# Kernel optimization log

Hardware: AMD Instinct MI355X
Metric: run time of the kernel (lower is better)

## Reference

```python
import jax, jax.numpy as jnp
import numpy as np

N = 100000
IN_DIM = 1280
HID = 128
EPS = 1e-5

def _gconv(x, src, dst, W, b, n):
    # DGL GraphConv, norm='both': D_out^{-1/2} gather -> sum -> D_in^{-1/2}, then W, b.
    # Project first (in_feats >= out_feats here) so edge messages are HID-dim.
    ones = jnp.ones(src.shape[0], dtype=x.dtype)
    out_deg = jnp.clip(jax.ops.segment_sum(ones, src, num_segments=n), 1.0)
    in_deg = jnp.clip(jax.ops.segment_sum(ones, dst, num_segments=n), 1.0)
    h = (x * (out_deg ** -0.5)[:, None]) @ W          # [n, HID]
    agg = jax.ops.segment_sum(h[src], dst, num_segments=n)  # scatter-add over edges
    return agg * (in_deg ** -0.5)[:, None] + b

def _batchnorm(x, g, b):
    m = x.mean(0)
    v = jnp.mean((x - m) ** 2, axis=0)  # biased variance (torch BN normalization)
    return (x - m) * jax.lax.rsqrt(v + EPS) * g + b

def _layer(x, edges, W, b, fcW, fcb, g, beta, n):
    # HeteroGraphConv aggregate='sum' over 3 relations, then FC + ReLU + BN
    h = _gconv(x, edges[0][0], edges[0][1], W[0], b[0], n)
    h = h + _gconv(x, edges[1][0], edges[1][1], W[1], b[1], n)
    h = h + _gconv(x, edges[2][0], edges[2][1], W[2], b[2], n)
    h = h @ fcW + fcb
    h = jax.nn.relu(h)
    return _batchnorm(h, g, beta)

def setup_inputs() -> dict:
    key = jax.random.key(0)
    ks = jax.random.split(key, 16)
    x = jax.random.normal(ks[0], (N, IN_DIM), dtype=jnp.float32)
    seq_edges = jax.random.randint(ks[1], (2, 200000), 0, N, dtype=jnp.int32)
    knn_edges = jax.random.randint(ks[2], (2, 1000000), 0, N, dtype=jnp.int32)
    dis_edges = jax.random.randint(ks[3], (2, 1600000), 0, N, dtype=jnp.int32)
    s_in = 1.0 / np.sqrt(IN_DIM)
    s_h = 1.0 / np.sqrt(HID)
    W0 = jax.random.normal(ks[4], (3, IN_DIM, HID), dtype=jnp.float32) * s_in
    b0 = jnp.zeros((3, HID), dtype=jnp.float32)
    fcW0 = jax.random.normal(ks[5], (HID, HID), dtype=jnp.float32) * s_h
    fcb0 = jnp.zeros((HID,), dtype=jnp.float32)
    g0 = jnp.ones((HID,), dtype=jnp.float32)
    beta0 = jnp.zeros((HID,), dtype=jnp.float32)
    W1 = jax.random.normal(ks[6], (3, HID, HID), dtype=jnp.float32) * s_h
    b1 = jnp.zeros((3, HID), dtype=jnp.float32)
    fcW1 = jax.random.normal(ks[7], (HID, HID), dtype=jnp.float32) * s_h
    fcb1 = jnp.zeros((HID,), dtype=jnp.float32)
    g1 = jnp.ones((HID,), dtype=jnp.float32)
    beta1 = jnp.zeros((HID,), dtype=jnp.float32)
    return {"x": x, "seq_edges": seq_edges, "knn_edges": knn_edges, "dis_edges": dis_edges,
            "W0": W0, "b0": b0, "fcW0": fcW0, "fcb0": fcb0, "g0": g0, "beta0": beta0,
            "W1": W1, "b1": b1, "fcW1": fcW1, "fcb1": fcb1, "g1": g1, "beta1": beta1}

def reference(x, seq_edges, knn_edges, dis_edges,
              W0, b0, fcW0, fcb0, g0, beta0,
              W1, b1, fcW1, fcb1, g1, beta1):
    edges = [seq_edges, knn_edges, dis_edges]
    n = x.shape[0]
    h = _layer(x, edges, W0, b0, fcW0, fcb0, g0, beta0, n)
    # dropout after non-final layers is identity at eval
    h = _layer(h, edges, W1, b1, fcW1, fcb1, g1, beta1, n)
    return h
```

## Files before the change

### kernel.cpp

```cpp
#include <hip/hip_runtime.h>
#include <hip/hip_bf16.h>
#include <math.h>

#define NN 100000
#define HID 128
#define EPSV 1e-5f

typedef short bf16x8 __attribute__((ext_vector_type(8)));
typedef float f32x4 __attribute__((ext_vector_type(4)));
typedef unsigned short u16;

__device__ __forceinline__ u16 f2b(float f) {
  unsigned u = __builtin_bit_cast(unsigned, f);
  u += 0x7FFFu + ((u >> 16) & 1u);
  return (u16)(u >> 16);
}
__device__ __forceinline__ float b2f(u16 h) {
  unsigned u = ((unsigned)h) << 16;
  return __builtin_bit_cast(float, u);
}

#define AS1(p) ((__attribute__((address_space(1))) void*)(p))
#define AS3(p) ((__attribute__((address_space(3))) void*)(p))


static __global__ void k_zero(float* __restrict__ p, int n) {
  int i = blockIdx.x * blockDim.x + threadIdx.x;
  if (i < n) p[i] = 0.f;
}

static __global__ void k_zero_i(int* __restrict__ p, int n) {
  int i = blockIdx.x * blockDim.x + threadIdx.x;
  if (i < n) p[i] = 0;
}

static __global__ void k_deg(const int* __restrict__ src, const int* __restrict__ dst,
                             int E, float* __restrict__ outdeg, float* __restrict__ indeg) {
  int e = blockIdx.x * blockDim.x + threadIdx.x;
  if (e < E) {
    atomicAdd(&outdeg[src[e]], 1.f);
    atomicAdd(&indeg[dst[e]], 1.f);
  }
}

static __global__ void k_counts(const float* __restrict__ indegRaw, int* __restrict__ counts, int n3) {
  int i = blockIdx.x * blockDim.x + threadIdx.x;
  if (i < n3) counts[i] = (int)indegRaw[i];
  else if (i == n3) counts[i] = 0;
}

static __global__ void k_rsqrt_clip(float* __restrict__ p, int n) {
  int i = blockIdx.x * blockDim.x + threadIdx.x;
  if (i < n) p[i] = rsqrtf(fmaxf(p[i], 1.f));
}

static __global__ void k_scan1(const int* __restrict__ in, int* __restrict__ out,
                               int* __restrict__ aux, int n) {
  __shared__ int s[256];
  int t = threadIdx.x, i = blockIdx.x * 256 + t;
  int v = (i < n) ? in[i] : 0;
  s[t] = v; __syncthreads();
#pragma unroll
  for (int d = 1; d < 256; d <<= 1) {
    int x = (t >= d) ? s[t - d] : 0;
    __syncthreads();
    s[t] += x;
    __syncthreads();
  }
  if (i < n) out[i] = s[t] - v;
  if (t == 255) aux[blockIdx.x] = s[255];
}

static __global__ void k_scan2(int* __restrict__ aux, int nb) {
  __shared__ int s[256];
  __shared__ int carry;
  int t = threadIdx.x;
  if (t == 0) carry = 0;
  __syncthreads();
  for (int base = 0; base < nb; base += 256) {
    int i = base + t;
    int v = (i < nb) ? aux[i] : 0;
    s[t] = v; __syncthreads();
#pragma unroll
    for (int d = 1; d < 256; d <<= 1) {
      int x = (t >= d) ? s[t - d] : 0;
      __syncthreads();
      s[t] += x;
      __syncthreads();
    }
    int excl = s[t] - v + carry;
    if (i < nb) aux[i] = excl;
    int tot = s[255];
    __syncthreads();
    if (t == 0) carry += tot;
    __syncthreads();
  }
}

static __global__ void k_scan3(int* __restrict__ out, const int* __restrict__ aux, int n) {
  int i = blockIdx.x * 256 + threadIdx.x;
  if (i < n) out[i] += aux[blockIdx.x];
}

static __global__ void k_fill(const int* __restrict__ src, const int* __restrict__ dst, int E,
                              const int* __restrict__ off, int* __restrict__ cur,
                              int rbase, int* __restrict__ srt) {
  int e = blockIdx.x * blockDim.x + threadIdx.x;
  if (e < E) {
    int d = dst[e];
    int p = off[rbase + d] + atomicAdd(&cur[rbase + d], 1);
    srt[p] = src[e];
  }
}

static __global__ void k_cvt_w(const float* __restrict__ W, u16* __restrict__ Wt, int K) {
  int i = blockIdx.x * blockDim.x + threadIdx.x;
  int tot = 3 * K * 128;
  if (i < tot) {
    int rel = i / (K * 128);
    int rem = i - rel * K * 128;
    int k = rem >> 7;
    int c = rem & 127;
    Wt[((size_t)rel * 128 + c) * K + k] = f2b(W[i]);
  }
}

static __global__ void k_cvt_fcw(const float* __restrict__ W, u16* __restrict__ Bt) {
  int i = blockIdx.x * blockDim.x + threadIdx.x;
  if (i < 128 * 128) {
    int k = i >> 7, c = i & 127;
    Bt[c * 128 + k] = f2b(W[i]);
  }
}

template<int K, bool AF32>
__global__ __launch_bounds__(256, 3)
void k_gemm2p(const void* __restrict__ Av,
              const u16* __restrict__ Wt,
              const float* __restrict__ sout,
              u16* __restrict__ Y,
              int M, int NT)
{
  constexpr int A_U16 = AF32 ? 8192 : 4096;
  constexpr int B_U16 = 4096;
  __shared__ u16 lds[2][A_U16 + B_U16];

  const int bid  = blockIdx.x;
  const int xcd  = bid & 7;
  const int s    = bid >> 3;
  const int rel  = s % 3;
  const int tile = xcd + 8 * (s / 3);
  if (tile >= NT) return;
  const int row0 = tile * 128;

  const int t    = threadIdx.x;
  const int lane = t & 63;
  const int w    = t >> 6;
  const int wm   = w >> 1, wn = w & 1;
  const int l15  = lane & 15, l4 = lane >> 4;
  const int kl   = l4 * 8;
  const int nk   = K / 32;

  const u16* Wr = Wt + (size_t)rel * 128 * K;

  int r0 = row0 + (2 * w) * 16 + l15;      if (r0 >= M) r0 = M - 1;
  int r1 = row0 + (2 * w + 1) * 16 + l15;  if (r1 >= M) r1 = M - 1;

  const u16* gb0 = Wr + (size_t)((2 * w) * 16 + l15) * K + kl;
  const u16* gb1 = Wr + (size_t)((2 * w + 1) * 16 + l15) * K + kl;

  const float* Af = (const float*)Av;
  const u16*   Ab = (const u16*)Av;

  auto STAGE = [&](int buf, int k0) {
    u16* L = &lds[buf][0];
    if constexpr (AF32) {
      const float* sa0 = Af + (size_t)r0 * K + k0 + kl;
      const float* sa1 = Af + (size_t)r1 * K + k0 + kl;
      __builtin_amdgcn_global_load_lds(AS1(sa0),     AS3(L + (2 * w) * 1024),       16, 0, 0);
      __builtin_amdgcn_global_load_lds(AS1(sa0 + 4), AS3(L + (2 * w) * 1024 + 512), 16, 0, 0);
      __builtin_amdgcn_global_load_lds(AS1(sa1),     AS3(L + (2 * w + 1) * 1024),       16, 0, 0);
      __builtin_amdgcn_global_load_lds(AS1(sa1 + 4), AS3(L + (2 * w + 1) * 1024 + 512), 16, 0, 0);
    } else {
      const u16* sa0 = Ab + (size_t)r0 * K + k0 + kl;
      const u16* sa1 = Ab + (size_t)r1 * K + k0 + kl;
      __builtin_amdgcn_global_load_lds(AS1(sa0), AS3(L + (2 * w) * 512),     16, 0, 0);
      __builtin_amdgcn_global_load_lds(AS1(sa1), AS3(L + (2 * w + 1) * 512), 16, 0, 0);
    }
    u16* Bd = L + A_U16;
    __builtin_amdgcn_global_load_lds(AS1(gb0 + k0), AS3(Bd + (2 * w) * 512),     16, 0, 0);
    __builtin_amdgcn_global_load_lds(AS1(gb1 + k0), AS3(Bd + (2 * w + 1) * 512), 16, 0, 0);
  };

  f32x4 acc[4][4];
#pragma unroll
  for (int m = 0; m < 4; ++m)
#pragma unroll
    for (int n = 0; n < 4; ++n) acc[m][n] = (f32x4){0.f, 0.f, 0.f, 0.f};

  STAGE(0, 0);

  for (int k = 0; k < nk; ++k) {
    asm volatile("s_waitcnt vmcnt(0)" ::: "memory");
    __builtin_amdgcn_sched_barrier(0);
    __builtin_amdgcn_s_barrier();
    __builtin_amdgcn_sched_barrier(0);

    if (k + 1 < nk) STAGE((k + 1) & 1, (k + 1) * 32);

    const int cur = k & 1;
    bf16x8 a[4], b[4];
    if constexpr (AF32) {
      const float* Al = (const float*)&lds[cur][0];
#pragma unroll
      for (int m = 0; m < 4; ++m) {
        f32x4 lo = *(const f32x4*)&Al[(wm * 4 + m) * 512 + lane * 4];
        f32x4 hi = *(const f32x4*)&Al[(wm * 4 + m) * 512 + 256 + lane * 4];
        union { bf16x8 v; u16 u[8]; } q;
#pragma unroll
        for (int j = 0; j < 4; ++j) {
          q.u[j]     = __builtin_bit_cast(u16, __float2bfloat16(lo[j]));
          q.u[4 + j] = __builtin_bit_cast(u16, __float2bfloat16(hi[j]));
        }
        a[m] = q.v;
      }
    } else {
      const u16* Al = &lds[cur][0];
#pragma unroll
      for (int m = 0; m < 4; ++m) a[m] = *(const bf16x8*)&Al[(wm * 4 + m) * 512 + lane * 8];
    }
    {
      const u16* Bl = &lds[cur][A_U16];
#pragma unroll
      for (int n = 0; n < 4; ++n) b[n] = *(const bf16x8*)&Bl[(wn * 4 + n) * 512 + lane * 8];
    }

#pragma unroll
    for (int m = 0; m < 4; ++m)
#pragma unroll
      for (int n = 0; n < 4; ++n)
        acc[m][n] = __builtin_amdgcn_mfma_f32_16x16x32_bf16(a[m], b[n], acc[m][n], 0, 0, 0);
  }

#pragma unroll
  for (int m = 0; m < 4; ++m) {
    const int rb = row0 + wm * 64 + m * 16 + l4 * 4;
#pragma unroll
    for (int j = 0; j < 4; ++j) {
      const int row = rb + j;
      if (row < M) {
        const float sc = sout[(size_t)rel * NN + row];
        u16* yp = Y + (size_t)row * 384 + rel * 128 + wn * 64 + l15;
#pragma unroll
        for (int n = 0; n < 4; ++n) yp[n * 16] = f2b(acc[m][n][j] * sc);
      }
    }
  }
}

static __global__ __launch_bounds__(256)
void k_gather(const int* __restrict__ off, const int* __restrict__ srt,
              const float* __restrict__ sin_, const u16* __restrict__ Y,
              const float* __restrict__ b, u16* __restrict__ acc16)
{
  int d = blockIdx.x * 4 + (threadIdx.x >> 6);
  if (d >= NN) return;
  int c = (threadIdx.x & 63) * 2;
  float v0 = b[c]     + b[128 + c]     + b[256 + c];
  float v1 = b[c + 1] + b[128 + c + 1] + b[256 + c + 1];
#pragma unroll
  for (int r = 0; r < 3; ++r) {
    int base = r * NN + d;
    int j0 = off[base], j1 = off[base + 1];
    float p0 = 0.f, p1 = 0.f;
    int j = j0;
    for (; j + 4 <= j1; j += 4) {
      int s0 = srt[j], s1 = srt[j + 1], s2 = srt[j + 2], s3 = srt[j + 3];
      unsigned u0 = *(const unsigned*)&Y[(size_t)s0 * 384 + r * 128 + c];
      unsigned u1 = *(const unsigned*)&Y[(size_t)s1 * 384 + r * 128 + c];
      unsigned u2 = *(const unsigned*)&Y[(size_t)s2 * 384 + r * 128 + c];
      unsigned u3 = *(const unsigned*)&Y[(size_t)s3 * 384 + r * 128 + c];
      p0 += b2f((u16)(u0 & 0xFFFFu)) + b2f((u16)(u1 & 0xFFFFu))
          + b2f((u16)(u2 & 0xFFFFu)) + b2f((u16)(u3 & 0xFFFFu));
      p1 += b2f((u16)(u0 >> 16)) + b2f((u16)(u1 >> 16))
          + b2f((u16)(u2 >> 16)) + b2f((u16)(u3 >> 16));
    }
    for (; j < j1; ++j) {
      int s = srt[j];
      unsigned u = *(const unsigned*)&Y[(size_t)s * 384 + r * 128 + c];
      p0 += b2f((u16)(u & 0xFFFFu));
      p1 += b2f((u16)(u >> 16));
    }
    float sc = sin_[base];
    v0 += p0 * sc;
    v1 += p1 * sc;
  }
  unsigned out = (unsigned)f2b(v0) | ((unsigned)f2b(v1) << 16);
  *(unsigned*)&acc16[(size_t)d * 128 + c] = out;
}

static __global__ __launch_bounds__(512)
void k_fc_mfma(const u16* __restrict__ A,
               const u16* __restrict__ Bt,
               const float* __restrict__ bias,
               float* __restrict__ Z, int M)
{
  __shared__ u16 Ab[4][4096];

  const int row0 = blockIdx.x * 128;
  const int t    = threadIdx.x;
  const int lane = t & 63;
  const int w    = t >> 6;
  const int wm   = w >> 2;
  const int wn   = w & 3;
  const int l15  = lane & 15, l4 = lane >> 4;
  const int kl   = l4 * 8;

  int ar = row0 + w * 16 + l15;  if (ar >= M) ar = M - 1;

  bf16x8 br[2][4];
#pragma unroll
  for (int n = 0; n < 2; ++n)
#pragma unroll
    for (int ks = 0; ks < 4; ++ks)
      br[n][ks] = *(const bf16x8*)&Bt[(size_t)(wn * 32 + n * 16 + l15) * 128 + ks * 32 + kl];

#pragma unroll
  for (int ks = 0; ks < 4; ++ks)
    __builtin_amdgcn_global_load_lds(AS1(A + (size_t)ar * 128 + ks * 32 + kl),
                                     AS3(&Ab[ks][w * 512]), 16, 0, 0);

  asm volatile("s_waitcnt vmcnt(0)" ::: "memory");
  __syncthreads();

  f32x4 acc[4][2];
#pragma unroll
  for (int m = 0; m < 4; ++m) { acc[m][0] = (f32x4){0,0,0,0}; acc[m][1] = (f32x4){0,0,0,0}; }

#pragma unroll
  for (int ks = 0; ks < 4; ++ks) {
#pragma unroll
    for (int m = 0; m < 4; ++m) {
      bf16x8 a = *(const bf16x8*)&Ab[ks][(wm * 4 + m) * 512 + lane * 8];
      acc[m][0] = __builtin_amdgcn_mfma_f32_16x16x32_bf16(a, br[0][ks], acc[m][0], 0, 0, 0);
      acc[m][1] = __builtin_amdgcn_mfma_f32_16x16x32_bf16(a, br[1][ks], acc[m][1], 0, 0, 0);
    }
  }

#pragma unroll
  for (int m = 0; m < 4; ++m) {
    const int rb = row0 + wm * 64 + m * 16 + l4 * 4;
#pragma unroll
    for (int j = 0; j < 4; ++j) {
      const int row = rb + j;
      if (row < M) {
#pragma unroll
        for (int n = 0; n < 2; ++n) {
          const int cc = wn * 32 + n * 16 + l15;
          Z[(size_t)row * 128 + cc] = fmaxf(acc[m][n][j] + bias[cc], 0.f);
        }
      }
    }
  }
}

static __global__ void k_bn_stats(const float* __restrict__ Z, int M, float* __restrict__ stats) {
  int col = threadIdx.x;
  float s = 0.f, s2 = 0.f;
  for (int row = blockIdx.x; row < M; row += gridDim.x) {
    float v = Z[(size_t)row * 128 + col];
    s += v;
    s2 += v * v;
  }
  atomicAdd(&stats[col], s);
  atomicAdd(&stats[128 + col], s2);
}

static __global__ void k_bn_finalize(const float* __restrict__ stats, int M,
                                     const float* __restrict__ g, const float* __restrict__ beta,
                                     float* __restrict__ ab) {
  int j = threadIdx.x;
  float m  = stats[j] / (float)M;
  float v  = stats[128 + j] / (float)M - m * m;
  float inv = rsqrtf(v + EPSV) * g[j];
  ab[j]       = inv;
  ab[128 + j] = beta[j] - m * inv;
}

template<bool OUT_BF16>
static __global__ void k_bn_apply(const float* __restrict__ Z, const float* __restrict__ ab,
                                  void* __restrict__ out, int n) {
  int i = blockIdx.x * blockDim.x + threadIdx.x;
  if (i < n) {
    int j = i & 127;
    float v = Z[i] * ab[j] + ab[128 + j];
    if constexpr (OUT_BF16) ((u16*)out)[i] = f2b(v);
    else                    ((float*)out)[i] = v;
  }
}


template<int K, bool AF32, bool OUT_BF16>
static void run_layer(const void* X,
                      const u16* Wt, const float* b,
                      const u16* fcWt, const float* fcb,
                      const float* g, const float* beta,
                      const int* off, const int* srt,
                      float* sOut, float* sIn, u16* Y, float* Z, u16* acc16,
                      float* stats, float* ab, void* out, hipStream_t stream)
{
  const int NT = (NN + 127) / 128;
  const int nblk = 24 * ((NT + 7) / 8);
  k_gemm2p<K, AF32><<<nblk, 256, 0, stream>>>(X, Wt, sOut, Y, NN, NT);

  k_gather<<<(NN + 3) / 4, 256, 0, stream>>>(off, srt, sIn, Y, b, acc16);

  k_fc_mfma<<<NT, 512, 0, stream>>>(acc16, fcWt, fcb, Z, NN);

  k_zero<<<1, 256, 0, stream>>>(stats, 256);
  k_bn_stats<<<1024, 128, 0, stream>>>(Z, NN, stats);
  k_bn_finalize<<<1, 128, 0, stream>>>(stats, NN, g, beta, ab);
  k_bn_apply<OUT_BF16><<<(NN * HID + 255) / 256, 256, 0, stream>>>(Z, ab, out, NN * HID);
}

extern "C" void kernel_launch(void* const* d_in, const int* in_sizes, int n_in,
                              void* d_out, int out_size, void* d_ws, size_t ws_size,
                              hipStream_t stream)
{
  const float* x    = (const float*)d_in[0];
  const int*   seq  = (const int*)d_in[1];
  const int*   knn  = (const int*)d_in[2];
  const int*   dis  = (const int*)d_in[3];
  const float* W0   = (const float*)d_in[4];
  const float* b0   = (const float*)d_in[5];
  const float* fcW0 = (const float*)d_in[6];
  const float* fcb0 = (const float*)d_in[7];
  const float* g0   = (const float*)d_in[8];
  const float* be0  = (const float*)d_in[9];
  const float* W1   = (const float*)d_in[10];
  const float* b1   = (const float*)d_in[11];
  const float* fcW1 = (const float*)d_in[12];
  const float* fcb1 = (const float*)d_in[13];
  const float* g1   = (const float*)d_in[14];
  const float* be1  = (const float*)d_in[15];

  const int E[3] = { in_sizes[1] / 2, in_sizes[2] / 2, in_sizes[3] / 2 };
  const int* srcs[3] = { seq, knn, dis };

  const size_t N = NN;
  const int M3 = 3 * NN;

  float* ws    = (float*)d_ws;
  float* sOut  = ws;
  float* sIn   = sOut + 3 * N;
  u16*   acc16 = (u16*)(sIn + 3 * N);
  float* accF  = (float*)acc16;
  float* stats = accF + N * 128;
  float* ab    = stats + 256;
  u16*   Y     = (u16*)(ab + 256);
  float* Z     = (float*)Y;
  u16*   h16   = Y + N * 384;
  u16*   Wt0   = h16 + N * 128;
  u16*   Wt1   = Wt0 + 3 * 128 * 1280;
  u16*   fcWt0 = Wt1 + 3 * 128 * 128;
  u16*   fcWt1 = fcWt0 + 128 * 128;
  int*   counts= (int*)(fcWt1 + 128 * 128);
  int*   off   = counts + (M3 + 1);
  int*   aux   = off + (M3 + 1);
  int*   cur   = aux + 1536;
  int*   srt   = cur + M3;

  k_cvt_w<<<(3 * 1280 * 128 + 255) / 256, 256, 0, stream>>>(W0, Wt0, 1280);
  k_cvt_w<<<(3 * 128 * 128 + 255) / 256, 256, 0, stream>>>(W1, Wt1, 128);
  k_cvt_fcw<<<(128 * 128 + 255) / 256, 256, 0, stream>>>(fcW0, fcWt0);
  k_cvt_fcw<<<(128 * 128 + 255) / 256, 256, 0, stream>>>(fcW1, fcWt1);

  k_zero<<<(6 * NN + 255) / 256, 256, 0, stream>>>(sOut, 6 * NN);
  for (int r = 0; r < 3; ++r) {
    k_deg<<<(E[r] + 255) / 256, 256, 0, stream>>>(
        srcs[r], srcs[r] + E[r], E[r], sOut + (size_t)r * N, sIn + (size_t)r * N);
  }
  k_counts<<<(M3 + 1 + 255) / 256, 256, 0, stream>>>(sIn, counts, M3);
  k_rsqrt_clip<<<(6 * NN + 255) / 256, 256, 0, stream>>>(sOut, 6 * NN);

  const int nsc = M3 + 1;
  const int nb  = (nsc + 255) / 256;
  k_scan1<<<nb, 256, 0, stream>>>(counts, off, aux, nsc);
  k_scan2<<<1, 256, 0, stream>>>(aux, nb);
  k_scan3<<<nb, 256, 0, stream>>>(off, aux, nsc);

  k_zero_i<<<(M3 + 255) / 256, 256, 0, stream>>>(cur, M3);
  for (int r = 0; r < 3; ++r) {
    k_fill<<<(E[r] + 255) / 256, 256, 0, stream>>>(
        srcs[r], srcs[r] + E[r], E[r], off, cur, r * NN, srt);
  }

  run_layer<1280, true, true>(x, Wt0, b0, fcWt0, fcb0, g0, be0, off, srt,
                              sOut, sIn, Y, Z, acc16, stats, ab, h16, stream);

  run_layer<128, false, false>(h16, Wt1, b1, fcWt1, fcb1, g1, be1, off, srt,
                               sOut, sIn, Y, Z, acc16, stats, ab, d_out, stream);
}
```

Measured before the change: 1.360 ms.

## Replace LDS-staged projection GEMM with register-direct global loads

```diff
diff --git a/kernel.cpp b/kernel.cpp
--- a/kernel.cpp
+++ b/kernel.cpp
@@ -134,22 +134,18 @@
 }
 
 template<int K, bool AF32>
-__global__ __launch_bounds__(256, 3)
-void k_gemm2p(const void* __restrict__ Av,
-              const u16* __restrict__ Wt,
-              const float* __restrict__ sout,
-              u16* __restrict__ Y,
-              int M, int NT)
+__global__ __launch_bounds__(256)
+void k_gemm_reg(const void* __restrict__ Av,
+                const u16* __restrict__ Wt,
+                const float* __restrict__ sout,
+                u16* __restrict__ Y,
+                int M, int NT)
 {
-  constexpr int A_U16 = AF32 ? 8192 : 4096;
-  constexpr int B_U16 = 4096;
-  __shared__ u16 lds[2][A_U16 + B_U16];
-
   const int bid  = blockIdx.x;
   const int xcd  = bid & 7;
-  const int s    = bid >> 3;
-  const int rel  = s % 3;
-  const int tile = xcd + 8 * (s / 3);
+  const int sidx = bid >> 3;
+  const int rel  = sidx % 3;
+  const int tile = xcd + 8 * (sidx / 3);
   if (tile >= NT) return;
   const int row0 = tile * 128;
 
@@ -158,88 +154,81 @@
   const int w    = t >> 6;
   const int wm   = w >> 1, wn = w & 1;
   const int l15  = lane & 15, l4 = lane >> 4;
-  const int kl   = l4 * 8;
   const int nk   = K / 32;
-
-  const u16* Wr = Wt + (size_t)rel * 128 * K;
-
-  int r0 = row0 + (2 * w) * 16 + l15;      if (r0 >= M) r0 = M - 1;
-  int r1 = row0 + (2 * w + 1) * 16 + l15;  if (r1 >= M) r1 = M - 1;
-
-  const u16* gb0 = Wr + (size_t)((2 * w) * 16 + l15) * K + kl;
-  const u16* gb1 = Wr + (size_t)((2 * w + 1) * 16 + l15) * K + kl;
 
   const float* Af = (const float*)Av;
   const u16*   Ab = (const u16*)Av;
-
-  auto STAGE = [&](int buf, int k0) {
-    u16* L = &lds[buf][0];
-    if constexpr (AF32) {
-      const float* sa0 = Af + (size_t)r0 * K + k0 + kl;
-      const float* sa1 = Af + (size_t)r1 * K + k0 + kl;
-      __builtin_amdgcn_global_load_lds(AS1(sa0),     AS3(L + (2 * w) * 1024),       16, 0, 0);
-      __builtin_amdgcn_global_load_lds(AS1(sa0 + 4), AS3(L + (2 * w) * 1024 + 512), 16, 0, 0);
-      __builtin_amdgcn_global_load_lds(AS1(sa1),     AS3(L + (2 * w + 1) * 1024),       16, 0, 0);
-      __builtin_amdgcn_global_load_lds(AS1(sa1 + 4), AS3(L + (2 * w + 1) * 1024 + 512), 16, 0, 0);
-    } else {
-      const u16* sa0 = Ab + (size_t)r0 * K + k0 + kl;
-      const u16* sa1 = Ab + (size_t)r1 * K + k0 + kl;
-      __builtin_amdgcn_global_load_lds(AS1(sa0), AS3(L + (2 * w) * 512),     16, 0, 0);
-      __builtin_amdgcn_global_load_lds(AS1(sa1), AS3(L + (2 * w + 1) * 512), 16, 0, 0);
-    }
-    u16* Bd = L + A_U16;
-    __builtin_amdgcn_global_load_lds(AS1(gb0 + k0), AS3(Bd + (2 * w) * 512),     16, 0, 0);
-    __builtin_amdgcn_global_load_lds(AS1(gb1 + k0), AS3(Bd + (2 * w + 1) * 512), 16, 0, 0);
+  const u16*   Wr = Wt + (size_t)rel * 128 * K;
+
+  const float* ap[4];
+  const u16*   abp[4];
+  const u16*   bp[4];
+#pragma unroll
+  for (int m = 0; m < 4; ++m) {
+    int r = row0 + wm * 64 + m * 16 + l15;
+    if (r >= M) r = M - 1;
+    if constexpr (AF32) ap[m]  = Af + (size_t)r * K + l4 * 8;
+    else                abp[m] = Ab + (size_t)r * K + l4 * 8;
+  }
+#pragma unroll
+  for (int n = 0; n < 4; ++n)
+    bp[n] = Wr + (size_t)(wn * 64 + n * 16 + l15) * K + l4 * 8;
+
+  f32x4 acc[4][4];
+#pragma unroll
+  for (int m = 0; m < 4; ++m)
+#pragma unroll
+    for (int n = 0; n < 4; ++n) acc[m][n] = (f32x4){0.f, 0.f, 0.f, 0.f};
+
+  f32x4  ra[4][2];
+  bf16x8 a_nx[4];
+  bf16x8 b_nx[4];
+  bf16x8 a_cu[4], b_cu[4];
+
+  auto LOAD = [&](int k0) {
+#pragma unroll
+    for (int m = 0; m < 4; ++m) {
+      if constexpr (AF32) {
+        ra[m][0] = *(const f32x4*)(ap[m] + k0);
+        ra[m][1] = *(const f32x4*)(ap[m] + k0 + 4);
+      } else {
+        a_nx[m] = *(const bf16x8*)(abp[m] + k0);
+      }
+    }
+#pragma unroll
+    for (int n = 0; n < 4; ++n) b_nx[n] = *(const bf16x8*)(bp[n] + k0);
   };
 
-  f32x4 acc[4][4];
-#pragma unroll
-  for (int m = 0; m < 4; ++m)
-#pragma unroll
-    for (int n = 0; n < 4; ++n) acc[m][n] = (f32x4){0.f, 0.f, 0.f, 0.f};
-
-  STAGE(0, 0);
+  auto CVT = [&]() {
+#pragma unroll
+    for (int m = 0; m < 4; ++m) {
+      if constexpr (AF32) {
+        union { bf16x8 v; u16 u[8]; } q;
+#pragma unroll
+        for (int j = 0; j < 4; ++j) {
+          q.u[j]     = __builtin_bit_cast(u16, __float2bfloat16(ra[m][0][j]));
+          q.u[4 + j] = __builtin_bit_cast(u16, __float2bfloat16(ra[m][1][j]));
+        }
+        a_cu[m] = q.v;
+      } else {
+        a_cu[m] = a_nx[m];
+      }
+    }
+#pragma unroll
+    for (int n = 0; n < 4; ++n) b_cu[n] = b_nx[n];
+  };
+
+  LOAD(0);
+  CVT();
 
   for (int k = 0; k < nk; ++k) {
-    asm volatile("s_waitcnt vmcnt(0)" ::: "memory");
-    __builtin_amdgcn_sched_barrier(0);
-    __builtin_amdgcn_s_barrier();
-    __builtin_amdgcn_sched_barrier(0);
-
-    if (k + 1 < nk) STAGE((k + 1) & 1, (k + 1) * 32);
-
-    const int cur = k & 1;
-    bf16x8 a[4], b[4];
-    if constexpr (AF32) {
-      const float* Al = (const float*)&lds[cur][0];
-#pragma unroll
-      for (int m = 0; m < 4; ++m) {
-        f32x4 lo = *(const f32x4*)&Al[(wm * 4 + m) * 512 + lane * 4];
-        f32x4 hi = *(const f32x4*)&Al[(wm * 4 + m) * 512 + 256 + lane * 4];
-        union { bf16x8 v; u16 u[8]; } q;
-#pragma unroll
-        for (int j = 0; j < 4; ++j) {
-          q.u[j]     = __builtin_bit_cast(u16, __float2bfloat16(lo[j]));
-          q.u[4 + j] = __builtin_bit_cast(u16, __float2bfloat16(hi[j]));
-        }
-        a[m] = q.v;
-      }
-    } else {
-      const u16* Al = &lds[cur][0];
-#pragma unroll
-      for (int m = 0; m < 4; ++m) a[m] = *(const bf16x8*)&Al[(wm * 4 + m) * 512 + lane * 8];
-    }
-    {
-      const u16* Bl = &lds[cur][A_U16];
-#pragma unroll
-      for (int n = 0; n < 4; ++n) b[n] = *(const bf16x8*)&Bl[(wn * 4 + n) * 512 + lane * 8];
-    }
-
+    if (k + 1 < nk) LOAD((k + 1) * 32);
 #pragma unroll
     for (int m = 0; m < 4; ++m)
 #pragma unroll
       for (int n = 0; n < 4; ++n)
-        acc[m][n] = __builtin_amdgcn_mfma_f32_16x16x32_bf16(a[m], b[n], acc[m][n], 0, 0, 0);
+        acc[m][n] = __builtin_amdgcn_mfma_f32_16x16x32_bf16(a_cu[m], b_cu[n], acc[m][n], 0, 0, 0);
+    if (k + 1 < nk) CVT();
   }
 
 #pragma unroll
@@ -411,7 +400,7 @@
 {
   const int NT = (NN + 127) / 128;
   const int nblk = 24 * ((NT + 7) / 8);
-  k_gemm2p<K, AF32><<<nblk, 256, 0, stream>>>(X, Wt, sOut, Y, NN, NT);
+  k_gemm_reg<K, AF32><<<nblk, 256, 0, stream>>>(X, Wt, sOut, Y, NN, NT);
 
   k_gather<<<(NN + 3) / 4, 256, 0, stream>>>(off, srt, sIn, Y, b, acc16);
 
```

New measurement: 1.583 ms. 16.4% more time.
